# Kernel tuning notes

Hardware: AMD Instinct MI355X
Metric: run time of the kernel (lower is better)

The kernel has to match this reference:

```python
import jax, jax.numpy as jnp
import numpy as np

N_TOTAL = 200000
DIM = 256
N_GRAPHS = 8192
N_ITERS = 6


def setup_inputs() -> dict:
    key = jax.random.key(0)
    k1, k2, k3, k4, k5, k6 = jax.random.split(key, 6)
    x = jax.random.normal(k1, (N_TOTAL, DIM), dtype=jnp.float32)
    batch = jnp.sort(jax.random.randint(k2, (N_TOTAL,), 0, N_GRAPHS)).astype(jnp.int32)
    bound = 1.0 / np.sqrt(DIM)
    W_ih = jax.random.uniform(k3, (4 * DIM, DIM), jnp.float32, -bound, bound)
    W_hh = jax.random.uniform(k4, (4 * DIM, DIM), jnp.float32, -bound, bound)
    b_ih = jax.random.uniform(k5, (4 * DIM,), jnp.float32, -bound, bound)
    b_hh = jax.random.uniform(k6, (4 * DIM,), jnp.float32, -bound, bound)
    return {"x": x, "batch": batch, "n_graphs": N_GRAPHS,
            "W_ih": W_ih, "W_hh": W_hh, "b_ih": b_ih, "b_hh": b_hh}


def _lstm_cell(inp, h, c, W_ih, W_hh, b_ih, b_hh):
    # PyTorch LSTMCell: gates ordered i, f, g, o
    gates = inp @ W_ih.T + b_ih + h @ W_hh.T + b_hh
    i, f, g, o = jnp.split(gates, 4, axis=-1)
    c_new = jax.nn.sigmoid(f) * c + jax.nn.sigmoid(i) * jnp.tanh(g)
    h_new = jax.nn.sigmoid(o) * jnp.tanh(c_new)
    return h_new, c_new


def reference(x, batch, n_graphs, W_ih, W_hh, b_ih, b_hh):
    dim = x.shape[1]
    h = jnp.zeros((n_graphs, dim), x.dtype)
    c = jnp.zeros((n_graphs, dim), x.dtype)
    readout = jnp.zeros((n_graphs, dim), x.dtype)
    for _ in range(N_ITERS):
        # attention scores per node: <x_v, q_{g(v)}>
        scores = jnp.sum(x * h[batch], axis=-1)  # (N,)
        # torch scatter_reduce_ amax with zero init includes the 0 -> max(seg_max, 0)
        seg_max = jax.ops.segment_max(scores, batch, num_segments=n_graphs,
                                      indices_are_sorted=True)
        seg_max = jnp.maximum(seg_max, 0.0)
        e = jnp.exp(scores - seg_max[batch])
        seg_sum = jax.ops.segment_sum(e, batch, num_segments=n_graphs,
                                      indices_are_sorted=True)
        w = e / (seg_sum[batch] + 1e-8)  # (N,)
        readout = jax.ops.segment_sum(x * w[:, None], batch, num_segments=n_graphs,
                                      indices_are_sorted=True)  # (G, dim)
        h, c = _lstm_cell(readout, h, c, W_ih, W_hh, b_ih, b_hh)
    return jnp.concatenate([h, readout], axis=-1)  # (G, 2*dim)
```

## Files before the change

### kernel.cpp

```cpp
#include <hip/hip_runtime.h>
#include <hip/hip_bf16.h>
#include <hip/hip_fp16.h>
#include <stdint.h>

#define DIM 256
#define NG 8192
#define KDIM 512
#define GDIM 1024
#define N_ITERS 6
#define GPB 32
#define NBLK (NG / GPB)
#define NTHR 512

typedef __hip_bfloat16 bf16;
typedef __attribute__((ext_vector_type(8))) short bf16x8;
typedef __attribute__((ext_vector_type(4))) float f32x4;
typedef __attribute__((ext_vector_type(8))) unsigned short u16x8;

__device__ __forceinline__ float fast_sigmoid(float v) {
    return 1.0f / (1.0f + __expf(-v));
}
__device__ __forceinline__ float fast_tanh(float v) {
    float e = __expf(2.0f * v);
    return (e - 1.0f) / (e + 1.0f);
}
__device__ __forceinline__ unsigned short f2bf(float v) {
    __hip_bfloat16 t = __float2bfloat16(v);
    unsigned short u; __builtin_memcpy(&u, &t, 2); return u;
}
__device__ __forceinline__ unsigned short f2h(float v) {
    __half t = __float2half_rn(v);
    unsigned short u; __builtin_memcpy(&u, &t, 2); return u;
}
__device__ __forceinline__ float h2f(unsigned short u) {
    __half t; __builtin_memcpy(&t, &u, 2);
    return __half2float(t);
}

struct SM {
    unsigned short Acat[GPB * KDIM];
    float h[GPB * DIM];
};

__global__ __launch_bounds__(256) void k_prep(const int* __restrict__ batch, int n_nodes,
        int* __restrict__ offs,
        const float* __restrict__ Wih, const float* __restrict__ Whh,
        const float* __restrict__ bih, const float* __restrict__ bhh,
        bf16* __restrict__ Wfrag, float* __restrict__ bsum) {
    const int idx = blockIdx.x * blockDim.x + threadIdx.x;
    if (idx < 64 * 16 * 64) {
        const int nfrag = idx >> 10;
        const int kstep = (idx >> 6) & 15;
        const int lane  = idx & 63;
        const int c  = nfrag * 16 + (lane & 15);
        const int k0 = kstep * 32 + (lane >> 4) * 8;
        const int d  = ((c >> 7) << 5) | (c & 31);
        const int gt = (c >> 5) & 3;
        const int jsrc = gt * DIM + d;
        u16x8 pk;
        #pragma unroll
        for (int j = 0; j < 8; ++j) {
            const int k = k0 + j;
            const float v = (k < DIM) ? Wih[(size_t)jsrc * DIM + k]
                                      : Whh[(size_t)jsrc * DIM + (k - DIM)];
            pk[j] = f2bf(v);
        }
        *(u16x8*)&Wfrag[(size_t)idx * 8] = pk;
    }
    if (idx < GDIM) {
        const int d  = ((idx >> 7) << 5) | (idx & 31);
        const int gt = (idx >> 5) & 3;
        const int jsrc = gt * DIM + d;
        bsum[idx] = bih[jsrc] + bhh[jsrc];
    }
    if (idx < n_nodes) {
        const int b  = batch[idx];
        const int bp = (idx == 0) ? -1 : batch[idx - 1];
        for (int g = bp + 1; g <= b; ++g) offs[g] = idx;
        if (idx == n_nodes - 1)
            for (int g = b + 1; g <= NG; ++g) offs[g] = n_nodes;
    }
}

template <bool FIRST, bool LAST>
__device__ __forceinline__ void att_phase(int w, int lane, int g0,
        const float* __restrict__ xf, unsigned short* __restrict__ xb,
        const int* __restrict__ offs, float* __restrict__ out,
        SM& sm, int nmax) {
    const int half = lane >> 5, hl = lane & 31;
    #pragma unroll 1
    for (int gi = 0; gi < 4; ++gi) {
        const int gl = (w << 2) + gi;
        const int g  = g0 + gl;
        const int start = offs[g], end = offs[g + 1];
        const int nb = (end - start + 7) >> 3;

        float4 curA[4], curB[4];
        u16x8  curP[4];
        #pragma unroll
        for (int j = 0; j < 4; ++j) {
            const int r = start + half + 2 * j;
            const size_t ap = (size_t)min(r, nmax) * DIM + hl * 8;
            if constexpr (FIRST) {
                curA[j] = *(const float4*)&xf[ap];
                curB[j] = *(const float4*)&xf[ap + 4];
            } else {
                curP[j] = *(const u16x8*)&xb[ap];
            }
        }

        float hreg[8];
        {
            const float4 a = *(const float4*)&sm.h[gl * DIM + hl * 8];
            const float4 b = *(const float4*)&sm.h[gl * DIM + hl * 8 + 4];
            hreg[0] = a.x; hreg[1] = a.y; hreg[2] = a.z; hreg[3] = a.w;
            hreg[4] = b.x; hreg[5] = b.y; hreg[6] = b.z; hreg[7] = b.w;
        }

        float m = 0.0f;
        float s = 0.0f;
        float racc[8] = {0, 0, 0, 0, 0, 0, 0, 0};

        #pragma unroll 1
        for (int b = 0; b < nb; ++b) {
            float4 nxtA[4], nxtB[4];
            u16x8  nxtP[4];
            #pragma unroll
            for (int j = 0; j < 4; ++j) {
                const int r = start + half + 2 * (4 * (b + 1) + j);
                const size_t ap = (size_t)min(r, nmax) * DIM + hl * 8;
                if constexpr (FIRST) {
                    nxtA[j] = *(const float4*)&xf[ap];
                    nxtB[j] = *(const float4*)&xf[ap + 4];
                } else {
                    nxtP[j] = *(const u16x8*)&xb[ap];
                }
            }
            float xv[4][8];
            float dt[4];
            #pragma unroll
            for (int j = 0; j < 4; ++j) {
                if constexpr (FIRST) {
                    xv[j][0] = curA[j].x; xv[j][1] = curA[j].y;
                    xv[j][2] = curA[j].z; xv[j][3] = curA[j].w;
                    xv[j][4] = curB[j].x; xv[j][5] = curB[j].y;
                    xv[j][6] = curB[j].z; xv[j][7] = curB[j].w;
                } else {
                    #pragma unroll
                    for (int i = 0; i < 8; ++i) xv[j][i] = h2f(curP[j][i]);
                }
                float d = 0.0f;
                #pragma unroll
                for (int i = 0; i < 8; ++i) d = fmaf(xv[j][i], hreg[i], d);
                dt[j] = d;
            }
            #pragma unroll
            for (int off = 16; off > 0; off >>= 1) {
                #pragma unroll
                for (int j = 0; j < 4; ++j) dt[j] += __shfl_xor(dt[j], off);
            }
            #pragma unroll
            for (int j = 0; j < 4; ++j) {
                const int r = start + half + 2 * (4 * b + j);
                const float d  = (r < end) ? dt[j] : -1e30f;
                const float mn = fmaxf(m, d);
                const float al = __expf(m - mn);
                const float e  = __expf(d - mn);
                s = s * al + e;
                #pragma unroll
                for (int i = 0; i < 8; ++i) racc[i] = fmaf(racc[i], al, e * xv[j][i]);
                m = mn;
                if constexpr (FIRST) {
                    if (r < end) {
                        u16x8 st;
                        #pragma unroll
                        for (int i = 0; i < 8; ++i) st[i] = f2h(xv[j][i]);
                        *(u16x8*)&xb[(size_t)r * DIM + hl * 8] = st;
                    }
                }
            }
            #pragma unroll
            for (int j = 0; j < 4; ++j) {
                if constexpr (FIRST) { curA[j] = nxtA[j]; curB[j] = nxtB[j]; }
                else                 { curP[j] = nxtP[j]; }
            }
        }

        const float mo = __shfl_xor(m, 32);
        const float M  = fmaxf(m, mo);
        const float am = __expf(m - M);
        s *= am;
        #pragma unroll
        for (int j = 0; j < 8; ++j) racc[j] *= am;
        s += __shfl_xor(s, 32);
        #pragma unroll
        for (int j = 0; j < 8; ++j) racc[j] += __shfl_xor(racc[j], 32);
        const float inv = 1.0f / (s + 1e-8f);
        if (half == 0) {
            u16x8 ob;
            #pragma unroll
            for (int j = 0; j < 8; ++j) ob[j] = f2bf(racc[j] * inv);
            unsigned off = (unsigned)(gl * 1024 + hl * 16);
            off ^= (unsigned)((gl & 7) << 4);
            *(u16x8*)((char*)sm.Acat + off) = ob;
        } else if (LAST) {
            float o[8];
            #pragma unroll
            for (int j = 0; j < 8; ++j) o[j] = racc[j] * inv;
            *(float4*)&out[(size_t)g * KDIM + DIM + hl * 8]     = make_float4(o[0], o[1], o[2], o[3]);
            *(float4*)&out[(size_t)g * KDIM + DIM + hl * 8 + 4] = make_float4(o[4], o[5], o[6], o[7]);
        }
    }
}

__global__ __launch_bounds__(NTHR, 2) void k_fused(const float* __restrict__ xf,
        unsigned short* __restrict__ xb, const int* __restrict__ offs,
        const bf16* __restrict__ Wfrag, const float* __restrict__ bsum,
        float* __restrict__ out, int n_nodes) {
    __shared__ SM sm;
    const int tid  = threadIdx.x;
    const int w    = tid >> 6, lane = tid & 63;
    const int g0   = blockIdx.x * GPB;
    const int nmax = n_nodes - 1;

    for (int i = tid; i < GPB * KDIM; i += NTHR) sm.Acat[i] = 0;
    for (int i = tid; i < GPB * DIM;  i += NTHR) sm.h[i] = 0.0f;

    float c_[2][2][4] = {};
    float bv[8];
    #pragma unroll
    for (int nf = 0; nf < 8; ++nf) bv[nf] = bsum[w * 128 + nf * 16 + (lane & 15)];

    __syncthreads();

    const bf16* wb = Wfrag + (size_t)w * 65536 + (size_t)lane * 8;

    for (int it = 0; it < N_ITERS; ++it) {
        if (it == 0)                att_phase<true,  false>(w, lane, g0, xf, xb, offs, out, sm, nmax);
        else if (it < N_ITERS - 1)  att_phase<false, false>(w, lane, g0, xf, xb, offs, out, sm, nmax);
        else                        att_phase<false, true >(w, lane, g0, xf, xb, offs, out, sm, nmax);
        __syncthreads();

        f32x4 acc[2][8] = {};
        const int r0 = lane & 15;
        bf16x8 bcur[8], bnxt[8];
        #pragma unroll
        for (int nf = 0; nf < 8; ++nf)
            bcur[nf] = *(const bf16x8*)&wb[(size_t)nf * 8192];
        #pragma unroll
        for (int kstep = 0; kstep < 16; ++kstep) {
            #pragma unroll
            for (int nf = 0; nf < 8; ++nf)
                bnxt[nf] = *(const bf16x8*)&wb[(size_t)nf * 8192 + ((kstep + 1) & 15) * 512];
            const unsigned o0 = (unsigned)(r0 * 1024 + kstep * 64 + (lane >> 4) * 16)
                              ^ (unsigned)((r0 & 7) << 4);
            const unsigned o1 = o0 + 16 * 1024;
            const bf16x8 a0 = *(const bf16x8*)((const char*)sm.Acat + o0);
            const bf16x8 a1 = *(const bf16x8*)((const char*)sm.Acat + o1);
            #pragma unroll
            for (int nf = 0; nf < 8; ++nf) {
                acc[0][nf] = __builtin_amdgcn_mfma_f32_16x16x32_bf16(a0, bcur[nf], acc[0][nf], 0, 0, 0);
                acc[1][nf] = __builtin_amdgcn_mfma_f32_16x16x32_bf16(a1, bcur[nf], acc[1][nf], 0, 0, 0);
            }
            #pragma unroll
            for (int nf = 0; nf < 8; ++nf) bcur[nf] = bnxt[nf];
        }
        __syncthreads();

        #pragma unroll
        for (int mf = 0; mf < 2; ++mf) {
            #pragma unroll
            for (int dhi = 0; dhi < 2; ++dhi) {
                const int d = w * 32 + dhi * 16 + (lane & 15);
                #pragma unroll
                for (int rr = 0; rr < 4; ++rr) {
                    const int row = mf * 16 + (lane >> 4) * 4 + rr;
                    const float gi = acc[mf][0 + dhi][rr] + bv[0 + dhi];
                    const float gf = acc[mf][2 + dhi][rr] + bv[2 + dhi];
                    const float gg = acc[mf][4 + dhi][rr] + bv[4 + dhi];
                    const float go = acc[mf][6 + dhi][rr] + bv[6 + dhi];
                    const float cn = fast_sigmoid(gf) * c_[mf][dhi][rr]
                                   + fast_sigmoid(gi) * fast_tanh(gg);
                    const float hn = fast_sigmoid(go) * fast_tanh(cn);
                    c_[mf][dhi][rr] = cn;
                    sm.h[row * DIM + d] = hn;
                    unsigned ho = (unsigned)(row * 1024 + (DIM + d) * 2)
                                ^ (unsigned)((row & 7) << 4);
                    *(unsigned short*)((char*)sm.Acat + ho) = f2bf(hn);
                }
            }
        }
        __syncthreads();
    }

    for (int i = tid; i < GPB * 64; i += NTHR) {
        const int row = i >> 6;
        const int dq  = (i & 63) << 2;
        *(float4*)&out[(size_t)(g0 + row) * KDIM + dq] = *(const float4*)&sm.h[row * DIM + dq];
    }
}

extern "C" void kernel_launch(void* const* d_in, const int* in_sizes, int n_in,
                              void* d_out, int out_size, void* d_ws, size_t ws_size,
                              hipStream_t stream) {
    const float* x     = (const float*)d_in[0];
    const int*   batch = (const int*)d_in[1];
    const float* Wih   = (const float*)d_in[3];
    const float* Whh   = (const float*)d_in[4];
    const float* bih   = (const float*)d_in[5];
    const float* bhh   = (const float*)d_in[6];
    const int n_nodes  = in_sizes[0] / DIM;
    float* out = (float*)d_out;

    char* ws = (char*)d_ws;
    size_t off = 0;
    auto alloc = [&](size_t bytes) -> void* {
        off = (off + 255) & ~(size_t)255;
        void* p = ws + off;
        off += bytes;
        return p;
    };
    int*   offs  = (int*)  alloc((size_t)(NG + 1) * sizeof(int));
    bf16*  Wfrag = (bf16*) alloc((size_t)GDIM * KDIM * sizeof(bf16));
    float* bsum  = (float*)alloc((size_t)GDIM * sizeof(float));
    unsigned short* xb = (unsigned short*)alloc((size_t)n_nodes * DIM * sizeof(unsigned short));
    (void)ws_size; (void)n_in; (void)out_size;

    const int cover = (n_nodes > 64 * 16 * 64) ? n_nodes : 64 * 16 * 64;
    const int pb = (cover + 255) / 256;

    k_prep<<<pb, 256, 0, stream>>>(batch, n_nodes, offs, Wih, Whh, bih, bhh, Wfrag, bsum);
    k_fused<<<NBLK, NTHR, 0, stream>>>(x, xb, offs, Wfrag, bsum, out, n_nodes);
}
```

Before: 914.9 us.

## Halve graphs per block, raise occupancy, and specialize zero-state first attention pass

Graphs per block drop from 32 to 16 (2 per wave), so each wave runs a single 16-row MFMA tile, and launch bounds rise to 4 blocks per SM. The first iteration exploits h=0: every score is zero, so the readout becomes a plain mean and the dot products, shuffles and exps are skipped while x is still converted to fp16. The GEMM loop now prefetches weight fragments in two halves of four to cut register pressure. The trade is twice as many blocks, each reloading the full weight matrix from global/L2 every iteration, which raises weight traffic.

```diff
diff --git a/kernel.cpp b/kernel.cpp
--- a/kernel.cpp
+++ b/kernel.cpp
@@ -8,9 +8,10 @@
 #define KDIM 512
 #define GDIM 1024
 #define N_ITERS 6
-#define GPB 32
+#define GPB 16
 #define NBLK (NG / GPB)
 #define NTHR 512
+#define GPW 2
 
 typedef __hip_bfloat16 bf16;
 typedef __attribute__((ext_vector_type(8))) short bf16x8;
@@ -82,120 +83,128 @@
     }
 }
 
-template <bool FIRST, bool LAST>
+template <int MODE>
 __device__ __forceinline__ void att_phase(int w, int lane, int g0,
         const float* __restrict__ xf, unsigned short* __restrict__ xb,
         const int* __restrict__ offs, float* __restrict__ out,
         SM& sm, int nmax) {
     const int half = lane >> 5, hl = lane & 31;
     #pragma unroll 1
-    for (int gi = 0; gi < 4; ++gi) {
-        const int gl = (w << 2) + gi;
+    for (int gi = 0; gi < GPW; ++gi) {
+        const int gl = w * GPW + gi;
         const int g  = g0 + gl;
         const int start = offs[g], end = offs[g + 1];
-        const int nb = (end - start + 7) >> 3;
-
-        float4 curA[4], curB[4];
-        u16x8  curP[4];
-        #pragma unroll
-        for (int j = 0; j < 4; ++j) {
-            const int r = start + half + 2 * j;
-            const size_t ap = (size_t)min(r, nmax) * DIM + hl * 8;
-            if constexpr (FIRST) {
+        const int n  = end - start;
+        const int nb = (n + 7) >> 3;
+        float racc[8] = {0, 0, 0, 0, 0, 0, 0, 0};
+        float s = 0.0f;
+
+        if constexpr (MODE == 0) {
+            float4 curA[4], curB[4];
+            #pragma unroll
+            for (int j = 0; j < 4; ++j) {
+                const int r = start + half + 2 * j;
+                const size_t ap = (size_t)min(r, nmax) * DIM + hl * 8;
                 curA[j] = *(const float4*)&xf[ap];
                 curB[j] = *(const float4*)&xf[ap + 4];
-            } else {
-                curP[j] = *(const u16x8*)&xb[ap];
-            }
-        }
-
-        float hreg[8];
-        {
-            const float4 a = *(const float4*)&sm.h[gl * DIM + hl * 8];
-            const float4 b = *(const float4*)&sm.h[gl * DIM + hl * 8 + 4];
-            hreg[0] = a.x; hreg[1] = a.y; hreg[2] = a.z; hreg[3] = a.w;
-            hreg[4] = b.x; hreg[5] = b.y; hreg[6] = b.z; hreg[7] = b.w;
-        }
-
-        float m = 0.0f;
-        float s = 0.0f;
-        float racc[8] = {0, 0, 0, 0, 0, 0, 0, 0};
-
-        #pragma unroll 1
-        for (int b = 0; b < nb; ++b) {
-            float4 nxtA[4], nxtB[4];
-            u16x8  nxtP[4];
-            #pragma unroll
-            for (int j = 0; j < 4; ++j) {
-                const int r = start + half + 2 * (4 * (b + 1) + j);
-                const size_t ap = (size_t)min(r, nmax) * DIM + hl * 8;
-                if constexpr (FIRST) {
+            }
+            #pragma unroll 1
+            for (int b = 0; b < nb; ++b) {
+                float4 nxtA[4], nxtB[4];
+                #pragma unroll
+                for (int j = 0; j < 4; ++j) {
+                    const int r = start + half + 2 * (4 * (b + 1) + j);
+                    const size_t ap = (size_t)min(r, nmax) * DIM + hl * 8;
                     nxtA[j] = *(const float4*)&xf[ap];
                     nxtB[j] = *(const float4*)&xf[ap + 4];
-                } else {
-                    nxtP[j] = *(const u16x8*)&xb[ap];
-                }
-            }
-            float xv[4][8];
-            float dt[4];
+                }
+                #pragma unroll
+                for (int j = 0; j < 4; ++j) {
+                    const int r = start + half + 2 * (4 * b + j);
+                    if (r < end) {
+                        racc[0] += curA[j].x; racc[1] += curA[j].y;
+                        racc[2] += curA[j].z; racc[3] += curA[j].w;
+                        racc[4] += curB[j].x; racc[5] += curB[j].y;
+                        racc[6] += curB[j].z; racc[7] += curB[j].w;
+                        u16x8 st;
+                        st[0] = f2h(curA[j].x); st[1] = f2h(curA[j].y);
+                        st[2] = f2h(curA[j].z); st[3] = f2h(curA[j].w);
+                        st[4] = f2h(curB[j].x); st[5] = f2h(curB[j].y);
+                        st[6] = f2h(curB[j].z); st[7] = f2h(curB[j].w);
+                        *(u16x8*)&xb[(size_t)r * DIM + hl * 8] = st;
+                    }
+                }
+                #pragma unroll
+                for (int j = 0; j < 4; ++j) { curA[j] = nxtA[j]; curB[j] = nxtB[j]; }
+            }
+            s = 0.0f;
+        } else {
+            float hreg[8];
+            {
+                const float4 a = *(const float4*)&sm.h[gl * DIM + hl * 8];
+                const float4 b = *(const float4*)&sm.h[gl * DIM + hl * 8 + 4];
+                hreg[0] = a.x; hreg[1] = a.y; hreg[2] = a.z; hreg[3] = a.w;
+                hreg[4] = b.x; hreg[5] = b.y; hreg[6] = b.z; hreg[7] = b.w;
+            }
+            u16x8 curP[4];
             #pragma unroll
             for (int j = 0; j < 4; ++j) {
-                if constexpr (FIRST) {
-                    xv[j][0] = curA[j].x; xv[j][1] = curA[j].y;
-                    xv[j][2] = curA[j].z; xv[j][3] = curA[j].w;
-                    xv[j][4] = curB[j].x; xv[j][5] = curB[j].y;
-                    xv[j][6] = curB[j].z; xv[j][7] = curB[j].w;
-                } else {
+                const int r = start + half + 2 * j;
+                curP[j] = *(const u16x8*)&xb[(size_t)min(r, nmax) * DIM + hl * 8];
+            }
+            float m = 0.0f;
+            #pragma unroll 1
+            for (int b = 0; b < nb; ++b) {
+                u16x8 nxtP[4];
+                #pragma unroll
+                for (int j = 0; j < 4; ++j) {
+                    const int r = start + half + 2 * (4 * (b + 1) + j);
+                    nxtP[j] = *(const u16x8*)&xb[(size_t)min(r, nmax) * DIM + hl * 8];
+                }
+                float xv[4][8];
+                float dt[4];
+                #pragma unroll
+                for (int j = 0; j < 4; ++j) {
                     #pragma unroll
                     for (int i = 0; i < 8; ++i) xv[j][i] = h2f(curP[j][i]);
-                }
-                float d = 0.0f;
-                #pragma unroll
-                for (int i = 0; i < 8; ++i) d = fmaf(xv[j][i], hreg[i], d);
-                dt[j] = d;
-            }
-            #pragma unroll
-            for (int off = 16; off > 0; off >>= 1) {
-                #pragma unroll
-                for (int j = 0; j < 4; ++j) dt[j] += __shfl_xor(dt[j], off);
-            }
-            #pragma unroll
-            for (int j = 0; j < 4; ++j) {
-                const int r = start + half + 2 * (4 * b + j);
-                const float d  = (r < end) ? dt[j] : -1e30f;
-                const float mn = fmaxf(m, d);
-                const float al = __expf(m - mn);
-                const float e  = __expf(d - mn);
-                s = s * al + e;
-                #pragma unroll
-                for (int i = 0; i < 8; ++i) racc[i] = fmaf(racc[i], al, e * xv[j][i]);
-                m = mn;
-                if constexpr (FIRST) {
-                    if (r < end) {
-                        u16x8 st;
-                        #pragma unroll
-                        for (int i = 0; i < 8; ++i) st[i] = f2h(xv[j][i]);
-                        *(u16x8*)&xb[(size_t)r * DIM + hl * 8] = st;
-                    }
-                }
-            }
-            #pragma unroll
-            for (int j = 0; j < 4; ++j) {
-                if constexpr (FIRST) { curA[j] = nxtA[j]; curB[j] = nxtB[j]; }
-                else                 { curP[j] = nxtP[j]; }
-            }
-        }
-
-        const float mo = __shfl_xor(m, 32);
-        const float M  = fmaxf(m, mo);
-        const float am = __expf(m - M);
-        s *= am;
-        #pragma unroll
-        for (int j = 0; j < 8; ++j) racc[j] *= am;
-        s += __shfl_xor(s, 32);
+                    float d = 0.0f;
+                    #pragma unroll
+                    for (int i = 0; i < 8; ++i) d = fmaf(xv[j][i], hreg[i], d);
+                    dt[j] = d;
+                }
+                #pragma unroll
+                for (int off = 16; off > 0; off >>= 1) {
+                    #pragma unroll
+                    for (int j = 0; j < 4; ++j) dt[j] += __shfl_xor(dt[j], off);
+                }
+                #pragma unroll
+                for (int j = 0; j < 4; ++j) {
+                    const int r = start + half + 2 * (4 * b + j);
+                    const float d  = (r < end) ? dt[j] : -1e30f;
+                    const float mn = fmaxf(m, d);
+                    const float al = __expf(m - mn);
+                    const float e  = __expf(d - mn);
+                    s = s * al + e;
+                    #pragma unroll
+                    for (int i = 0; i < 8; ++i) racc[i] = fmaf(racc[i], al, e * xv[j][i]);
+                    m = mn;
+                }
+                #pragma unroll
+                for (int j = 0; j < 4; ++j) curP[j] = nxtP[j];
+            }
+            const float mo = __shfl_xor(m, 32);
+            const float M  = fmaxf(m, mo);
+            const float am = __expf(m - M);
+            s *= am;
+            #pragma unroll
+            for (int j = 0; j < 8; ++j) racc[j] *= am;
+        }
+
+        if constexpr (MODE != 0) s += __shfl_xor(s, 32);
         #pragma unroll
         for (int j = 0; j < 8; ++j) racc[j] += __shfl_xor(racc[j], 32);
-        const float inv = 1.0f / (s + 1e-8f);
+        const float inv = (MODE == 0) ? 1.0f / ((float)n + 1e-8f)
+                                      : 1.0f / (s + 1e-8f);
         if (half == 0) {
             u16x8 ob;
             #pragma unroll
@@ -203,7 +212,7 @@
             unsigned off = (unsigned)(gl * 1024 + hl * 16);
             off ^= (unsigned)((gl & 7) << 4);
             *(u16x8*)((char*)sm.Acat + off) = ob;
-        } else if (LAST) {
+        } else if (MODE == 2) {
             float o[8];
             #pragma unroll
             for (int j = 0; j < 8; ++j) o[j] = racc[j] * inv;
@@ -213,7 +222,7 @@
     }
 }
 
-__global__ __launch_bounds__(NTHR, 2) void k_fused(const float* __restrict__ xf,
+__global__ __launch_bounds__(NTHR, 4) void k_fused(const float* __restrict__ xf,
         unsigned short* __restrict__ xb, const int* __restrict__ offs,
         const bf16* __restrict__ Wfrag, const float* __restrict__ bsum,
         float* __restrict__ out, int n_nodes) {
@@ -226,7 +235,7 @@
     for (int i = tid; i < GPB * KDIM; i += NTHR) sm.Acat[i] = 0;
     for (int i = tid; i < GPB * DIM;  i += NTHR) sm.h[i] = 0.0f;
 
-    float c_[2][2][4] = {};
+    float c_[2][4] = {};
     float bv[8];
     #pragma unroll
     for (int nf = 0; nf < 8; ++nf) bv[nf] = bsum[w * 128 + nf * 16 + (lane & 15)];
@@ -236,58 +245,55 @@
     const bf16* wb = Wfrag + (size_t)w * 65536 + (size_t)lane * 8;
 
     for (int it = 0; it < N_ITERS; ++it) {
-        if (it == 0)                att_phase<true,  false>(w, lane, g0, xf, xb, offs, out, sm, nmax);
-        else if (it < N_ITERS - 1)  att_phase<false, false>(w, lane, g0, xf, xb, offs, out, sm, nmax);
-        else                        att_phase<false, true >(w, lane, g0, xf, xb, offs, out, sm, nmax);
+        if (it == 0)                att_phase<0>(w, lane, g0, xf, xb, offs, out, sm, nmax);
+        else if (it < N_ITERS - 1)  att_phase<1>(w, lane, g0, xf, xb, offs, out, sm, nmax);
+        else                        att_phase<2>(w, lane, g0, xf, xb, offs, out, sm, nmax);
         __syncthreads();
 
-        f32x4 acc[2][8] = {};
+        f32x4 acc[8] = {};
         const int r0 = lane & 15;
-        bf16x8 bcur[8], bnxt[8];
-        #pragma unroll
-        for (int nf = 0; nf < 8; ++nf)
-            bcur[nf] = *(const bf16x8*)&wb[(size_t)nf * 8192];
+        bf16x8 bA[4], bB[4];
+        #pragma unroll
+        for (int q = 0; q < 4; ++q) bA[q] = *(const bf16x8*)&wb[(size_t)q * 8192];
+        #pragma unroll
+        for (int q = 0; q < 4; ++q) bB[q] = *(const bf16x8*)&wb[(size_t)(q + 4) * 8192];
         #pragma unroll
         for (int kstep = 0; kstep < 16; ++kstep) {
-            #pragma unroll
-            for (int nf = 0; nf < 8; ++nf)
-                bnxt[nf] = *(const bf16x8*)&wb[(size_t)nf * 8192 + ((kstep + 1) & 15) * 512];
             const unsigned o0 = (unsigned)(r0 * 1024 + kstep * 64 + (lane >> 4) * 16)
                               ^ (unsigned)((r0 & 7) << 4);
-            const unsigned o1 = o0 + 16 * 1024;
-            const bf16x8 a0 = *(const bf16x8*)((const char*)sm.Acat + o0);
-            const bf16x8 a1 = *(const bf16x8*)((const char*)sm.Acat + o1);
-            #pragma unroll
-            for (int nf = 0; nf < 8; ++nf) {
-                acc[0][nf] = __builtin_amdgcn_mfma_f32_16x16x32_bf16(a0, bcur[nf], acc[0][nf], 0, 0, 0);
-                acc[1][nf] = __builtin_amdgcn_mfma_f32_16x16x32_bf16(a1, bcur[nf], acc[1][nf], 0, 0, 0);
-            }
-            #pragma unroll
-            for (int nf = 0; nf < 8; ++nf) bcur[nf] = bnxt[nf];
+            const bf16x8 a = *(const bf16x8*)((const char*)sm.Acat + o0);
+            const int kn = ((kstep + 1) & 15) * 512;
+            #pragma unroll
+            for (int q = 0; q < 4; ++q)
+                acc[q] = __builtin_amdgcn_mfma_f32_16x16x32_bf16(a, bA[q], acc[q], 0, 0, 0);
+            #pragma unroll
+            for (int q = 0; q < 4; ++q) bA[q] = *(const bf16x8*)&wb[(size_t)q * 8192 + kn];
+            #pragma unroll
+            for (int q = 0; q < 4; ++q)
+                acc[4 + q] = __builtin_amdgcn_mfma_f32_16x16x32_bf16(a, bB[q], acc[4 + q], 0, 0, 0);
+            #pragma unroll
+            for (int q = 0; q < 4; ++q) bB[q] = *(const bf16x8*)&wb[(size_t)(q + 4) * 8192 + kn];
         }
         __syncthreads();
 
         #pragma unroll
-        for (int mf = 0; mf < 2; ++mf) {
-            #pragma unroll
-            for (int dhi = 0; dhi < 2; ++dhi) {
-                const int d = w * 32 + dhi * 16 + (lane & 15);
-                #pragma unroll
-                for (int rr = 0; rr < 4; ++rr) {
-                    const int row = mf * 16 + (lane >> 4) * 4 + rr;
-                    const float gi = acc[mf][0 + dhi][rr] + bv[0 + dhi];
-                    const float gf = acc[mf][2 + dhi][rr] + bv[2 + dhi];
-                    const float gg = acc[mf][4 + dhi][rr] + bv[4 + dhi];
-                    const float go = acc[mf][6 + dhi][rr] + bv[6 + dhi];
-                    const float cn = fast_sigmoid(gf) * c_[mf][dhi][rr]
-                                   + fast_sigmoid(gi) * fast_tanh(gg);
-                    const float hn = fast_sigmoid(go) * fast_tanh(cn);
-                    c_[mf][dhi][rr] = cn;
-                    sm.h[row * DIM + d] = hn;
-                    unsigned ho = (unsigned)(row * 1024 + (DIM + d) * 2)
-                                ^ (unsigned)((row & 7) << 4);
-                    *(unsigned short*)((char*)sm.Acat + ho) = f2bf(hn);
-                }
+        for (int dhi = 0; dhi < 2; ++dhi) {
+            const int d = w * 32 + dhi * 16 + (lane & 15);
+            #pragma unroll
+            for (int rr = 0; rr < 4; ++rr) {
+                const int row = (lane >> 4) * 4 + rr;
+                const float gi_ = acc[0 + dhi][rr] + bv[0 + dhi];
+                const float gf_ = acc[2 + dhi][rr] + bv[2 + dhi];
+                const float gg_ = acc[4 + dhi][rr] + bv[4 + dhi];
+                const float go_ = acc[6 + dhi][rr] + bv[6 + dhi];
+                const float cn = fast_sigmoid(gf_) * c_[dhi][rr]
+                               + fast_sigmoid(gi_) * fast_tanh(gg_);
+                const float hn = fast_sigmoid(go_) * fast_tanh(cn);
+                c_[dhi][rr] = cn;
+                sm.h[row * DIM + d] = hn;
+                unsigned ho = (unsigned)(row * 1024 + (DIM + d) * 2)
+                            ^ (unsigned)((row & 7) << 4);
+                *(unsigned short*)((char*)sm.Acat + ho) = f2bf(hn);
             }
         }
         __syncthreads();
```

After: 1.214 ms. +32.7%, slower.
